# Kernel tuning notes

Hardware: AMD Instinct MI355X
Metric: run time of the kernel (lower is better)

Reference implementation:

```python
import jax, jax.numpy as jnp
import numpy as np

B, T, F = 128, 512, 64
H, OUT, NUM_LAYERS = 1024, 64, 2


def _lstm_layer(x, W_ih, W_hh, b_ih, b_hh):
    # x: [B, T, Fin]; W_ih: [4H, Fin]; W_hh: [4H, H]; b_*: [4H]
    # PyTorch gate order: i, f, g, o
    Bsz = x.shape[0]
    Hd = W_hh.shape[1]
    # Precompute input contribution for all timesteps: [B, T, 4H]
    xg = jnp.einsum('btf,gf->btg', x, W_ih) + b_ih + b_hh

    def step(carry, xg_t):
        h, c = carry
        g = xg_t + h @ W_hh.T  # [B, 4H]
        i, f, gg, o = jnp.split(g, 4, axis=-1)
        i = jax.nn.sigmoid(i)
        f = jax.nn.sigmoid(f)
        gg = jnp.tanh(gg)
        o = jax.nn.sigmoid(o)
        c = f * c + i * gg
        h = o * jnp.tanh(c)
        return (h, c), h

    h0 = jnp.zeros((Bsz, Hd), dtype=x.dtype)
    c0 = jnp.zeros((Bsz, Hd), dtype=x.dtype)
    _, hs = jax.lax.scan(step, (h0, c0), jnp.swapaxes(xg, 0, 1))  # hs: [T, B, H]
    return jnp.swapaxes(hs, 0, 1)  # [B, T, H]


def setup_inputs() -> dict:
    key = jax.random.key(0)
    ks = jax.random.split(key, 12)
    s_in = 1.0 / np.sqrt(H)
    inp = {
        'input_batch': jax.random.normal(ks[0], (B, T, F), dtype=jnp.float32),
        'W_ih0': jax.random.uniform(ks[1], (4 * H, F), minval=-s_in, maxval=s_in),
        'W_hh0': jax.random.uniform(ks[2], (4 * H, H), minval=-s_in, maxval=s_in),
        'b_ih0': jax.random.uniform(ks[3], (4 * H,), minval=-s_in, maxval=s_in),
        'b_hh0': jax.random.uniform(ks[4], (4 * H,), minval=-s_in, maxval=s_in),
        'W_ih1': jax.random.uniform(ks[5], (4 * H, H), minval=-s_in, maxval=s_in),
        'W_hh1': jax.random.uniform(ks[6], (4 * H, H), minval=-s_in, maxval=s_in),
        'b_ih1': jax.random.uniform(ks[7], (4 * H,), minval=-s_in, maxval=s_in),
        'b_hh1': jax.random.uniform(ks[8], (4 * H,), minval=-s_in, maxval=s_in),
        'W_fc': jax.random.uniform(ks[9], (OUT, H), minval=-s_in, maxval=s_in),
        'b_fc': jax.random.uniform(ks[10], (OUT,), minval=-s_in, maxval=s_in),
    }
    return inp


def reference(input_batch, W_ih0, W_hh0, b_ih0, b_hh0, W_ih1, W_hh1, b_ih1, b_hh1, W_fc, b_fc):
    # The per-timestep python loop with carried (h, c) is mathematically a full
    # sequence pass through the stacked LSTM, with the Linear applied at every step.
    h1 = _lstm_layer(input_batch, W_ih0, W_hh0, b_ih0, b_hh0)  # [B, T, H]
    h2 = _lstm_layer(h1, W_ih1, W_hh1, b_ih1, b_hh1)           # [B, T, H]
    preds = jnp.einsum('bth,oh->bto', h2, W_fc) + b_fc          # [B, T, OUT]
    return preds
```

## Files before the change

kernel.cpp:

```cpp
#include <hip/hip_runtime.h>
#include <hip/hip_bf16.h>

typedef __bf16 bf16_t;
typedef bf16_t bf16x8 __attribute__((ext_vector_type(8)));
typedef float f32x4 __attribute__((ext_vector_type(4)));
typedef unsigned long long u64;

#define T_SEQ 512
#define NB 128
#define HID 1024
#define FIN 64
#define HB (NB * HID)
#define NBLK 256
#define DM 32
#define DX 8
#define X1SLOT (4096 * NB)

#define NF0 136
#define NF1 128
#define NFR 64
#define L0_STAGE (NF0 * 64 * 8)
#define L1_STAGE (NFR * 64 * 8)
#define LDS_BYTES 151552

#define F0 0
#define FX 64
#define F1 128
#define SYNC_N 256

__device__ __forceinline__ float sigm_f(float x) { return 1.0f / (1.0f + __expf(-x)); }
__device__ __forceinline__ float tanh_f(float x) { return 2.0f * sigm_f(2.0f * x) - 1.0f; }

__device__ __forceinline__ unsigned ldcnt(const unsigned* p) {
    return __hip_atomic_load(p, __ATOMIC_RELAXED, __HIP_MEMORY_SCOPE_AGENT);
}
__device__ __forceinline__ void stw32(unsigned* p, unsigned v) {
    __hip_atomic_store(p, v, __ATOMIC_RELAXED, __HIP_MEMORY_SCOPE_AGENT);
}
__device__ __forceinline__ void stwf(float* p, float v) {
    __hip_atomic_store(p, v, __ATOMIC_RELAXED, __HIP_MEMORY_SCOPE_AGENT);
}
__device__ __forceinline__ void stw64(u64* p, u64 v) {
    __hip_atomic_store(p, v, __ATOMIC_RELAXED, __HIP_MEMORY_SCOPE_AGENT);
}


__global__ __launch_bounds__(256) void prep_kernel(
    const float* __restrict__ x,
    const float* __restrict__ Wih0, const float* __restrict__ Whh0,
    const float* __restrict__ bih0, const float* __restrict__ bhh0,
    const float* __restrict__ Wih1, const float* __restrict__ Whh1,
    const float* __restrict__ bih1, const float* __restrict__ bhh1,
    const float* __restrict__ Wfc,
    bf16_t* __restrict__ Wf0, bf16_t* __restrict__ Wf1, bf16_t* __restrict__ WfR,
    bf16_t* __restrict__ xswz, bf16_t* __restrict__ Wfcb,
    float* __restrict__ bias0, float* __restrict__ bias1,
    bf16_t* __restrict__ mh0, bf16_t* __restrict__ mh1,
    unsigned* __restrict__ sync)
{
    const unsigned stride = gridDim.x * blockDim.x;
    const unsigned i0 = blockIdx.x * blockDim.x + threadIdx.x;

    for (unsigned i = i0; i < SYNC_N; i += stride) sync[i] = 0u;

    for (unsigned i = i0; i < 64u * NF0 * 64u; i += stride) {
        unsigned g0 = i / (NF0 * 64u), rem = i % (NF0 * 64u);
        unsigned f = rem >> 6, ln = rem & 63u;
        unsigned pc = f >> 2, mt = f & 3u;
        unsigned r = mt * 16u + (ln & 15u);
        unsigned row = (r & 3u) * HID + g0 * 16u + (r >> 2);
        unsigned k0 = pc * 32u + (ln >> 4) * 8u;
        bf16_t* dst = Wf0 + (size_t)i * 8;
#pragma unroll
        for (int e = 0; e < 8; ++e) {
            unsigned k = k0 + e;
            float v = (k < FIN) ? Wih0[(size_t)row * FIN + k]
                                : Whh0[(size_t)row * HID + (k - FIN)];
            dst[e] = (bf16_t)v;
        }
    }
    for (unsigned i = i0; i < 64u * NF1 * 64u; i += stride) {
        unsigned g = i >> 13, rem = i & 8191u;
        unsigned f = rem >> 6, ln = rem & 63u;
        unsigned pc = f >> 2, mt = f & 3u;
        unsigned r = mt * 16u + (ln & 15u);
        unsigned row = (r & 3u) * HID + g * 16u + (r >> 2);
        unsigned k0 = pc * 32u + (ln >> 4) * 8u;
        bf16_t* dst = Wf1 + (size_t)i * 8;
#pragma unroll
        for (int e = 0; e < 8; ++e)
            dst[e] = (bf16_t)Wih1[(size_t)row * HID + k0 + e];
    }
    for (unsigned i = i0; i < 128u * NFR * 64u; i += stride) {
        unsigned g1 = i >> 12, rem = i & 4095u;
        unsigned f = rem >> 6, ln = rem & 63u;
        unsigned pc = f >> 1, mt = f & 1u;
        unsigned r = mt * 16u + (ln & 15u);
        unsigned row = (r & 3u) * HID + g1 * 8u + (r >> 2);
        unsigned k0 = pc * 32u + (ln >> 4) * 8u;
        bf16_t* dst = WfR + (size_t)i * 8;
#pragma unroll
        for (int e = 0; e < 8; ++e)
            dst[e] = (bf16_t)Whh1[(size_t)row * HID + k0 + e];
    }
    for (unsigned i = i0; i < 4194304u; i += stride) {
        unsigned e = i & 7u, unit = i >> 3;
        unsigned lane = unit & 63u, g = unit >> 6;
        unsigned wvv = g & 7u, pt = g >> 3;
        unsigned p = pt & 1u, t = pt >> 1;
        unsigned n = wvv * 16u + (lane & 15u);
        unsigned k = p * 32u + (lane >> 4) * 8u + e;
        xswz[i] = (bf16_t)x[((size_t)n * T_SEQ + t) * FIN + k];
    }
    for (unsigned i = i0; i < 64u * HID; i += stride)
        Wfcb[i] = (bf16_t)Wfc[i];
    for (unsigned i = i0; i < (unsigned)(DM * HB); i += stride) {
        mh0[i] = (bf16_t)0.0f; mh1[i] = (bf16_t)0.0f;
    }
    for (unsigned i = i0; i < 4096u; i += stride) {
        bias0[i] = bih0[i] + bhh0[i];
        bias1[i] = bih1[i] + bhh1[i];
    }
}

__global__ __launch_bounds__(512) void lstm_persist(
    const bf16_t* __restrict__ Wf0, const bf16_t* __restrict__ Wf1,
    const bf16_t* __restrict__ WfR,
    const float* __restrict__ bias0, const float* __restrict__ bias1,
    const bf16_t* __restrict__ xswz,
    bf16_t* __restrict__ mh0, bf16_t* __restrict__ mh1,
    bf16_t* __restrict__ h2buf,
    float* __restrict__ x1r,
    unsigned* __restrict__ sync)
{
    extern __shared__ bf16_t Wl[];
    const int b = blockIdx.x;
    const int tid = threadIdx.x;
    const int wv = tid >> 6;
    const int lane = tid & 63;
    const int q = lane >> 4;
    const int l = lane & 15;

    if (b < 64) {
        const int g0 = b;
        const int mh = wv >> 2, nh = wv & 3;
        const int nt0 = nh * 2, nt1 = nh * 2 + 1;
        for (int c = tid; c < NF0 * 64; c += 512)
            *(bf16x8*)(Wl + (size_t)c * 8) =
                *(const bf16x8*)(Wf0 + ((size_t)g0 * (NF0 * 64) + c) * 8);
        bf16_t* stage = Wl + L0_STAGE;
        float* cl = (float*)(Wl + L0_STAGE + 2048);
        for (int i = tid; i < 16 * NB; i += 512) cl[i] = 0.0f;
        float bj[2][4];
#pragma unroll
        for (int mti = 0; mti < 2; ++mti) {
            const int j = g0 * 16 + (mh * 2 + mti) * 4 + q;
#pragma unroll
            for (int gg = 0; gg < 4; ++gg) bj[mti][gg] = bias0[gg * HID + j];
        }
        __syncthreads();

        for (int t = 0; t < T_SEQ; ++t) {
            f32x4 acc[2][2] = {{{0.f,0.f,0.f,0.f},{0.f,0.f,0.f,0.f}},
                               {{0.f,0.f,0.f,0.f},{0.f,0.f,0.f,0.f}}};
            {
                const bf16_t* X = xswz + (size_t)t * 8192;
#pragma unroll
                for (int p = 0; p < 2; ++p) {
                    bf16x8 av0 = *(const bf16x8*)(Wl + ((size_t)(p * 4 + mh * 2) * 64 + lane) * 8);
                    bf16x8 av1 = *(const bf16x8*)(Wl + ((size_t)(p * 4 + mh * 2 + 1) * 64 + lane) * 8);
                    bf16x8 bv0 = *(const bf16x8*)(X + (((size_t)p * 8 + nt0) * 64 + lane) * 8);
                    bf16x8 bv1 = *(const bf16x8*)(X + (((size_t)p * 8 + nt1) * 64 + lane) * 8);
                    acc[0][0] = __builtin_amdgcn_mfma_f32_16x16x32_bf16(av0, bv0, acc[0][0], 0, 0, 0);
                    acc[0][1] = __builtin_amdgcn_mfma_f32_16x16x32_bf16(av0, bv1, acc[0][1], 0, 0, 0);
                    acc[1][0] = __builtin_amdgcn_mfma_f32_16x16x32_bf16(av1, bv0, acc[1][0], 0, 0, 0);
                    acc[1][1] = __builtin_amdgcn_mfma_f32_16x16x32_bf16(av1, bv1, acc[1][1], 0, 0, 0);
                }
            }
            if (wv == 0) {
                const unsigned tA = (unsigned)t;
                const unsigned tB = (t >= DM) ? (unsigned)(t - (DM - 1)) : 0u;
                for (;;) {
                    bool ok = (ldcnt(&sync[F0 + lane]) >= tA)
                           && (ldcnt(&sync[FX + lane]) >= tB);
                    if (__all(ok)) break;
                    __builtin_amdgcn_s_sleep(1);
                }
            }
            __syncthreads();
            {
                const bf16_t* B = mh0 + (size_t)((t + DM - 1) & (DM - 1)) * HB;
                bf16x8 bb0[8], bb1[8];
#pragma unroll
                for (int i = 0; i < 8; ++i) {
                    bb0[i] = *(const bf16x8*)(B + (((size_t)i * 8 + nt0) * 64 + lane) * 8);
                    bb1[i] = *(const bf16x8*)(B + (((size_t)i * 8 + nt1) * 64 + lane) * 8);
                }
#pragma unroll
                for (int p = 0; p < 32; ++p) {
                    bf16x8 av0 = *(const bf16x8*)(Wl + ((size_t)((2 + p) * 4 + mh * 2) * 64 + lane) * 8);
                    bf16x8 av1 = *(const bf16x8*)(Wl + ((size_t)((2 + p) * 4 + mh * 2 + 1) * 64 + lane) * 8);
                    acc[0][0] = __builtin_amdgcn_mfma_f32_16x16x32_bf16(av0, bb0[p & 7], acc[0][0], 0, 0, 0);
                    acc[0][1] = __builtin_amdgcn_mfma_f32_16x16x32_bf16(av0, bb1[p & 7], acc[0][1], 0, 0, 0);
                    acc[1][0] = __builtin_amdgcn_mfma_f32_16x16x32_bf16(av1, bb0[p & 7], acc[1][0], 0, 0, 0);
                    acc[1][1] = __builtin_amdgcn_mfma_f32_16x16x32_bf16(av1, bb1[p & 7], acc[1][1], 0, 0, 0);
                    if (p + 8 < 32) {
                        bb0[p & 7] = *(const bf16x8*)(B + (((size_t)(p + 8) * 8 + nt0) * 64 + lane) * 8);
                        bb1[p & 7] = *(const bf16x8*)(B + (((size_t)(p + 8) * 8 + nt1) * 64 + lane) * 8);
                    }
                }
            }
#pragma unroll
            for (int mti = 0; mti < 2; ++mti) {
                const int u = (mh * 2 + mti) * 4 + q;
#pragma unroll
                for (int nti = 0; nti < 2; ++nti) {
                    const int n = (nh * 2 + nti) * 16 + l;
                    float iv = sigm_f(acc[mti][nti][0] + bj[mti][0]);
                    float fv = sigm_f(acc[mti][nti][1] + bj[mti][1]);
                    float gv = tanh_f(acc[mti][nti][2] + bj[mti][2]);
                    float ov = sigm_f(acc[mti][nti][3] + bj[mti][3]);
                    float cn = fv * cl[u * NB + n] + iv * gv;
                    cl[u * NB + n] = cn;
                    stage[n * 16 + u] = (bf16_t)(ov * tanh_f(cn));
                }
            }
            __syncthreads();
            if (tid < 256) {
                const int n = tid >> 1, half = tid & 1;
                u64 v0 = *(const u64*)(stage + n * 16 + half * 8);
                u64 v1 = *(const u64*)(stage + n * 16 + half * 8 + 4);
                size_t unit = ((size_t)((g0 >> 1) * 8 + (n >> 4))) * 64
                              + ((g0 & 1) * 2 + half) * 16 + (n & 15);
                u64* dst = (u64*)(mh0 + (size_t)(t & (DM - 1)) * HB) + unit * 2;
                stw64(dst, v0); stw64(dst + 1, v1);
            }
            __syncthreads();
            if (tid == 0) stw32(&sync[F0 + g0], (unsigned)(t + 1));
        }
    } else if (b < 128) {
        const int g = b - 64;
        const int mh = wv >> 2, nh = wv & 3;
        const int nt0 = nh * 2, nt1 = nh * 2 + 1;
        for (int c = tid; c < NF1 * 64; c += 512)
            *(bf16x8*)(Wl + (size_t)c * 8) =
                *(const bf16x8*)(Wf1 + ((size_t)g * (NF1 * 64) + c) * 8);
        __syncthreads();

        for (int t = 0; t < T_SEQ; ++t) {
            if (wv == 0) {
                const unsigned tA = (unsigned)(t + 1);
                const unsigned tC = (t >= DX) ? (unsigned)(t - (DX - 1)) : 0u;
                for (;;) {
                    bool ok = (ldcnt(&sync[F0 + lane]) >= tA)
                           && (ldcnt(&sync[F1 + lane]) >= tC)
                           && (ldcnt(&sync[F1 + 64 + lane]) >= tC);
                    if (__all(ok)) break;
                    __builtin_amdgcn_s_sleep(1);
                }
            }
            __syncthreads();
            f32x4 acc[2][2] = {{{0.f,0.f,0.f,0.f},{0.f,0.f,0.f,0.f}},
                               {{0.f,0.f,0.f,0.f},{0.f,0.f,0.f,0.f}}};
            {
                const bf16_t* B = mh0 + (size_t)(t & (DM - 1)) * HB;
                bf16x8 bb0[8], bb1[8];
#pragma unroll
                for (int i = 0; i < 8; ++i) {
                    bb0[i] = *(const bf16x8*)(B + (((size_t)i * 8 + nt0) * 64 + lane) * 8);
                    bb1[i] = *(const bf16x8*)(B + (((size_t)i * 8 + nt1) * 64 + lane) * 8);
                }
#pragma unroll
                for (int p = 0; p < 32; ++p) {
                    bf16x8 av0 = *(const bf16x8*)(Wl + ((size_t)(p * 4 + mh * 2) * 64 + lane) * 8);
                    bf16x8 av1 = *(const bf16x8*)(Wl + ((size_t)(p * 4 + mh * 2 + 1) * 64 + lane) * 8);
                    acc[0][0] = __builtin_amdgcn_mfma_f32_16x16x32_bf16(av0, bb0[p & 7], acc[0][0], 0, 0, 0);
                    acc[0][1] = __builtin_amdgcn_mfma_f32_16x16x32_bf16(av0, bb1[p & 7], acc[0][1], 0, 0, 0);
                    acc[1][0] = __builtin_amdgcn_mfma_f32_16x16x32_bf16(av1, bb0[p & 7], acc[1][0], 0, 0, 0);
                    acc[1][1] = __builtin_amdgcn_mfma_f32_16x16x32_bf16(av1, bb1[p & 7], acc[1][1], 0, 0, 0);
                    if (p + 8 < 32) {
                        bb0[p & 7] = *(const bf16x8*)(B + (((size_t)(p + 8) * 8 + nt0) * 64 + lane) * 8);
                        bb1[p & 7] = *(const bf16x8*)(B + (((size_t)(p + 8) * 8 + nt1) * 64 + lane) * 8);
                    }
                }
            }
            {
                float* P = x1r + (size_t)(t & (DX - 1)) * X1SLOT + (size_t)g * 64 * NB;
#pragma unroll
                for (int mti = 0; mti < 2; ++mti) {
                    const int u = (mh * 2 + mti) * 4 + q;
#pragma unroll
                    for (int nti = 0; nti < 2; ++nti) {
                        const int n = (nh * 2 + nti) * 16 + l;
#pragma unroll
                        for (int jj = 0; jj < 4; ++jj)
                            stwf(P + (size_t)(u * 4 + jj) * NB + n, acc[mti][nti][jj]);
                    }
                }
            }
            __syncthreads();
            if (tid == 0) stw32(&sync[FX + g], (unsigned)(t + 1));
        }
    } else {
        const int g1 = b - 128;
        const int nn = wv * 16 + l;
        for (int c = tid; c < NFR * 64; c += 512)
            *(bf16x8*)(Wl + (size_t)c * 8) =
                *(const bf16x8*)(WfR + ((size_t)g1 * (NFR * 64) + c) * 8);
        bf16_t* stage = Wl + L1_STAGE;
        float* cl = (float*)(Wl + L1_STAGE + 1024);
        for (int i = tid; i < 8 * NB; i += 512) cl[i] = 0.0f;
        float bj[2][4];
#pragma unroll
        for (int mt = 0; mt < 2; ++mt) {
            const int j = g1 * 8 + mt * 4 + q;
#pragma unroll
            for (int gg = 0; gg < 4; ++gg) bj[mt][gg] = bias1[gg * HID + j];
        }
        __syncthreads();

        for (int t = 0; t < T_SEQ; ++t) {
            if (wv == 0) {
                const unsigned tA = (unsigned)(t + 1);
                const unsigned tO = (unsigned)t;
                const unsigned gx = (unsigned)(g1 >> 1);
                for (;;) {
                    bool ok = (ldcnt(&sync[FX + gx]) >= tA)
                           && (ldcnt(&sync[F1 + lane]) >= tO)
                           && (ldcnt(&sync[F1 + 64 + lane]) >= tO);
                    if (__all(ok)) break;
                    __builtin_amdgcn_s_sleep(1);
                }
            }
            __syncthreads();
            float pv[2][4];
            {
                const float* P = x1r + (size_t)(t & (DX - 1)) * X1SLOT + (size_t)g1 * 32 * NB;
#pragma unroll
                for (int mt = 0; mt < 2; ++mt)
#pragma unroll
                    for (int jj = 0; jj < 4; ++jj)
                        pv[mt][jj] = P[(size_t)((mt * 4 + q) * 4 + jj) * NB + nn];
            }
            f32x4 acc[2] = {{0.f,0.f,0.f,0.f},{0.f,0.f,0.f,0.f}};
            {
                const bf16_t* B1 = mh1 + (size_t)((t + DM - 1) & (DM - 1)) * HB;
                bf16x8 bb[16];
#pragma unroll
                for (int i = 0; i < 16; ++i)
                    bb[i] = *(const bf16x8*)(B1 + (((size_t)i * 8 + wv) * 64 + lane) * 8);
#pragma unroll
                for (int p = 0; p < 32; ++p) {
                    bf16x8 bv = bb[p & 15];
#pragma unroll
                    for (int mt = 0; mt < 2; ++mt) {
                        bf16x8 av = *(const bf16x8*)(Wl + ((size_t)(p * 2 + mt) * 64 + lane) * 8);
                        acc[mt] = __builtin_amdgcn_mfma_f32_16x16x32_bf16(av, bv, acc[mt], 0, 0, 0);
                    }
                    if (p + 16 < 32)
                        bb[p & 15] = *(const bf16x8*)(B1 + (((size_t)(p + 16) * 8 + wv) * 64 + lane) * 8);
                }
            }
#pragma unroll
            for (int mt = 0; mt < 2; ++mt) {
                const int u = mt * 4 + q;
                float iv = sigm_f(acc[mt][0] + pv[mt][0] + bj[mt][0]);
                float fv = sigm_f(acc[mt][1] + pv[mt][1] + bj[mt][1]);
                float gv = tanh_f(acc[mt][2] + pv[mt][2] + bj[mt][2]);
                float ov = sigm_f(acc[mt][3] + pv[mt][3] + bj[mt][3]);
                float cn = fv * cl[u * NB + nn] + iv * gv;
                cl[u * NB + nn] = cn;
                stage[nn * 8 + u] = (bf16_t)(ov * tanh_f(cn));
            }
            __asm__ volatile("s_waitcnt lgkmcnt(0)" ::: "memory");
            u64 v = 0;
            if (q < 2) {
                v = *(const u64*)(stage + (size_t)(wv * 16 + l) * 8 + q * 4);
                size_t unit = ((size_t)(g1 >> 2) * 8 + wv) * 64 + (size_t)(g1 & 3) * 16 + l;
                stw64((u64*)(mh1 + (size_t)(t & (DM - 1)) * HB) + unit * 2 + q, v);
            }
            __syncthreads();
            if (tid == 0) stw32(&sync[F1 + g1], (unsigned)(t + 1));
            if (q < 2)
                *(u64*)(h2buf + ((size_t)(wv * 16 + l) * T_SEQ + t) * HID + g1 * 8 + q * 4) = v;
        }
    }
}

__global__ __launch_bounds__(256) void fc_kernel(
    const bf16_t* __restrict__ h2buf, const bf16_t* __restrict__ Wfcb,
    const float* __restrict__ bfc, float* __restrict__ out)
{
    const int tid = threadIdx.x, wv = tid >> 6, lane = tid & 63;
    const int q = lane >> 4, l = lane & 15;
    const int m0 = blockIdx.x * 64 + wv * 16;
    const bf16_t* arow = h2buf + (size_t)(m0 + l) * HID + q * 8;
    const bf16_t* brow = Wfcb + (size_t)l * HID + q * 8;
    f32x4 acc[4] = {{0.f,0.f,0.f,0.f},{0.f,0.f,0.f,0.f},{0.f,0.f,0.f,0.f},{0.f,0.f,0.f,0.f}};
#pragma unroll 4
    for (int p = 0; p < 32; ++p) {
        bf16x8 av = *(const bf16x8*)(arow + p * 32);
#pragma unroll
        for (int ntile = 0; ntile < 4; ++ntile) {
            bf16x8 bv = *(const bf16x8*)(brow + (size_t)ntile * 16 * HID + p * 32);
            acc[ntile] = __builtin_amdgcn_mfma_f32_16x16x32_bf16(av, bv, acc[ntile], 0, 0, 0);
        }
    }
#pragma unroll
    for (int ntile = 0; ntile < 4; ++ntile) {
        float bv = bfc[ntile * 16 + l];
#pragma unroll
        for (int r = 0; r < 4; ++r)
            out[(size_t)(m0 + q * 4 + r) * 64 + ntile * 16 + l] = acc[ntile][r] + bv;
    }
}

extern "C" void kernel_launch(void* const* d_in, const int* in_sizes, int n_in,
                              void* d_out, int out_size, void* d_ws, size_t ws_size,
                              hipStream_t stream)
{
    const float* x    = (const float*)d_in[0];
    const float* Wih0 = (const float*)d_in[1];
    const float* Whh0 = (const float*)d_in[2];
    const float* bih0 = (const float*)d_in[3];
    const float* bhh0 = (const float*)d_in[4];
    const float* Wih1 = (const float*)d_in[5];
    const float* Whh1 = (const float*)d_in[6];
    const float* bih1 = (const float*)d_in[7];
    const float* bhh1 = (const float*)d_in[8];
    const float* Wfc  = (const float*)d_in[9];
    const float* bfc  = (const float*)d_in[10];
    float* out = (float*)d_out;

    char* ws = (char*)d_ws;
    size_t off = 0;
    auto alloc = [&](size_t bytes) -> void* {
        void* p = ws + off;
        off += (bytes + 255) & ~(size_t)255;
        return p;
    };
    bf16_t* Wf0  = (bf16_t*)alloc((size_t)64 * NF0 * 64 * 8 * 2);
    bf16_t* Wf1  = (bf16_t*)alloc((size_t)64 * NF1 * 64 * 8 * 2);
    bf16_t* WfR  = (bf16_t*)alloc((size_t)128 * NFR * 64 * 8 * 2);
    bf16_t* xswz = (bf16_t*)alloc((size_t)NB * T_SEQ * FIN * 2);
    bf16_t* h2buf= (bf16_t*)alloc((size_t)NB * T_SEQ * HID * 2);
    bf16_t* mh0  = (bf16_t*)alloc((size_t)DM * HB * 2);
    bf16_t* mh1  = (bf16_t*)alloc((size_t)DM * HB * 2);
    float*  x1r  = (float*)alloc((size_t)DX * X1SLOT * 4);
    float*  bias0= (float*)alloc(4096 * 4);
    float*  bias1= (float*)alloc(4096 * 4);
    bf16_t* Wfcb = (bf16_t*)alloc((size_t)64 * HID * 2);
    unsigned* syncp = (unsigned*)alloc(SYNC_N * 4);
    if (off > ws_size) return;

    hipFuncSetAttribute((const void*)lstm_persist,
                        hipFuncAttributeMaxDynamicSharedMemorySize, LDS_BYTES);

    prep_kernel<<<1024, 256, 0, stream>>>(x, Wih0, Whh0, bih0, bhh0,
                                          Wih1, Whh1, bih1, bhh1, Wfc,
                                          Wf0, Wf1, WfR, xswz, Wfcb,
                                          bias0, bias1, mh0, mh1, syncp);

    void* args[] = { (void*)&Wf0, (void*)&Wf1, (void*)&WfR,
                     (void*)&bias0, (void*)&bias1,
                     (void*)&xswz, (void*)&mh0, (void*)&mh1,
                     (void*)&h2buf, (void*)&x1r,
                     (void*)&syncp };
    hipLaunchCooperativeKernel((void*)lstm_persist, dim3(NBLK), dim3(512),
                               args, LDS_BYTES, stream);

    fc_kernel<<<(NB * T_SEQ) / 64, 256, 0, stream>>>(h2buf, Wfcb, bfc, out);
}
```

Measured before the change: 4.817 ms.

## Split batch into two independent half-chunks pipelined through the persistent LSTM

```diff
diff --git a/kernel.cpp b/kernel.cpp
--- a/kernel.cpp
+++ b/kernel.cpp
@@ -10,11 +10,11 @@
 #define NB 128
 #define HID 1024
 #define FIN 64
-#define HB (NB * HID)
+#define HBH (64 * 1024)
 #define NBLK 256
 #define DM 32
 #define DX 8
-#define X1SLOT (4096 * NB)
+#define X1SLOTH (4096 * 64)
 
 #define NF0 136
 #define NF1 128
@@ -23,10 +23,7 @@
 #define L1_STAGE (NFR * 64 * 8)
 #define LDS_BYTES 151552
 
-#define F0 0
-#define FX 64
-#define F1 128
-#define SYNC_N 256
+#define SYNC_N 512
 
 __device__ __forceinline__ float sigm_f(float x) { return 1.0f / (1.0f + __expf(-x)); }
 __device__ __forceinline__ float tanh_f(float x) { return 2.0f * sigm_f(2.0f * x) - 1.0f; }
@@ -106,15 +103,14 @@
     for (unsigned i = i0; i < 4194304u; i += stride) {
         unsigned e = i & 7u, unit = i >> 3;
         unsigned lane = unit & 63u, g = unit >> 6;
-        unsigned wvv = g & 7u, pt = g >> 3;
-        unsigned p = pt & 1u, t = pt >> 1;
-        unsigned n = wvv * 16u + (lane & 15u);
+        unsigned nt = g & 3u, p = (g >> 2) & 1u, c = (g >> 3) & 1u, t = g >> 4;
+        unsigned n = c * 64u + nt * 16u + (lane & 15u);
         unsigned k = p * 32u + (lane >> 4) * 8u + e;
         xswz[i] = (bf16_t)x[((size_t)n * T_SEQ + t) * FIN + k];
     }
     for (unsigned i = i0; i < 64u * HID; i += stride)
         Wfcb[i] = (bf16_t)Wfc[i];
-    for (unsigned i = i0; i < (unsigned)(DM * HB); i += stride) {
+    for (unsigned i = i0; i < (unsigned)(2 * DM * HBH); i += stride) {
         mh0[i] = (bf16_t)0.0f; mh1[i] = (bf16_t)0.0f;
     }
     for (unsigned i = i0; i < 4096u; i += stride) {
@@ -123,7 +119,7 @@
     }
 }
 
-__global__ __launch_bounds__(512) void lstm_persist(
+__global__ __launch_bounds__(512, 2) void lstm_persist(
     const bf16_t* __restrict__ Wf0, const bf16_t* __restrict__ Wf1,
     const bf16_t* __restrict__ WfR,
     const float* __restrict__ bias0, const float* __restrict__ bias1,
@@ -140,16 +136,16 @@
     const int lane = tid & 63;
     const int q = lane >> 4;
     const int l = lane & 15;
+    const int mh = wv >> 2;
+    const int nh = wv & 3;
 
     if (b < 64) {
         const int g0 = b;
-        const int mh = wv >> 2, nh = wv & 3;
-        const int nt0 = nh * 2, nt1 = nh * 2 + 1;
-        for (int c = tid; c < NF0 * 64; c += 512)
-            *(bf16x8*)(Wl + (size_t)c * 8) =
-                *(const bf16x8*)(Wf0 + ((size_t)g0 * (NF0 * 64) + c) * 8);
+        for (int cc = tid; cc < NF0 * 64; cc += 512)
+            *(bf16x8*)(Wl + (size_t)cc * 8) =
+                *(const bf16x8*)(Wf0 + ((size_t)g0 * (NF0 * 64) + cc) * 8);
         bf16_t* stage = Wl + L0_STAGE;
-        float* cl = (float*)(Wl + L0_STAGE + 2048);
+        float* cl = (float*)(Wl + L0_STAGE + 1024);
         for (int i = tid; i < 16 * NB; i += 512) cl[i] = 0.0f;
         float bj[2][4];
 #pragma unroll
@@ -161,228 +157,212 @@
         __syncthreads();
 
         for (int t = 0; t < T_SEQ; ++t) {
-            f32x4 acc[2][2] = {{{0.f,0.f,0.f,0.f},{0.f,0.f,0.f,0.f}},
-                               {{0.f,0.f,0.f,0.f},{0.f,0.f,0.f,0.f}}};
-            {
-                const bf16_t* X = xswz + (size_t)t * 8192;
-#pragma unroll
-                for (int p = 0; p < 2; ++p) {
-                    bf16x8 av0 = *(const bf16x8*)(Wl + ((size_t)(p * 4 + mh * 2) * 64 + lane) * 8);
-                    bf16x8 av1 = *(const bf16x8*)(Wl + ((size_t)(p * 4 + mh * 2 + 1) * 64 + lane) * 8);
-                    bf16x8 bv0 = *(const bf16x8*)(X + (((size_t)p * 8 + nt0) * 64 + lane) * 8);
-                    bf16x8 bv1 = *(const bf16x8*)(X + (((size_t)p * 8 + nt1) * 64 + lane) * 8);
-                    acc[0][0] = __builtin_amdgcn_mfma_f32_16x16x32_bf16(av0, bv0, acc[0][0], 0, 0, 0);
-                    acc[0][1] = __builtin_amdgcn_mfma_f32_16x16x32_bf16(av0, bv1, acc[0][1], 0, 0, 0);
-                    acc[1][0] = __builtin_amdgcn_mfma_f32_16x16x32_bf16(av1, bv0, acc[1][0], 0, 0, 0);
-                    acc[1][1] = __builtin_amdgcn_mfma_f32_16x16x32_bf16(av1, bv1, acc[1][1], 0, 0, 0);
-                }
+#pragma unroll
+            for (int c = 0; c < 2; ++c) {
+                f32x4 acc[2] = {{0.f,0.f,0.f,0.f},{0.f,0.f,0.f,0.f}};
+                {
+                    const bf16_t* X = xswz + (size_t)(t * 2 + c) * 4096;
+#pragma unroll
+                    for (int p = 0; p < 2; ++p) {
+                        bf16x8 bv  = *(const bf16x8*)(X + (((size_t)p * 4 + nh) * 64 + lane) * 8);
+                        bf16x8 av0 = *(const bf16x8*)(Wl + ((size_t)(p * 4 + mh * 2) * 64 + lane) * 8);
+                        bf16x8 av1 = *(const bf16x8*)(Wl + ((size_t)(p * 4 + mh * 2 + 1) * 64 + lane) * 8);
+                        acc[0] = __builtin_amdgcn_mfma_f32_16x16x32_bf16(av0, bv, acc[0], 0, 0, 0);
+                        acc[1] = __builtin_amdgcn_mfma_f32_16x16x32_bf16(av1, bv, acc[1], 0, 0, 0);
+                    }
+                }
+                if (wv == 0) {
+                    const unsigned tA = (unsigned)t;
+                    const unsigned tB = (t >= DM) ? (unsigned)(t - (DM - 1)) : 0u;
+                    const unsigned* f0c = sync + c * 64;
+                    const unsigned* fxc = sync + 128 + c * 64;
+                    for (;;) {
+                        bool ok = (ldcnt(&f0c[lane]) >= tA) && (ldcnt(&fxc[lane]) >= tB);
+                        if (__all(ok)) break;
+                        __builtin_amdgcn_s_sleep(1);
+                    }
+                }
+                __syncthreads();
+                {
+                    const bf16_t* B = mh0 + ((size_t)c * DM + ((t + DM - 1) & (DM - 1))) * HBH;
+                    bf16x8 bb[16];
+#pragma unroll
+                    for (int i = 0; i < 16; ++i)
+                        bb[i] = *(const bf16x8*)(B + (((size_t)i * 4 + nh) * 64 + lane) * 8);
+#pragma unroll
+                    for (int p = 0; p < 32; ++p) {
+                        bf16x8 av0 = *(const bf16x8*)(Wl + ((size_t)((2 + p) * 4 + mh * 2) * 64 + lane) * 8);
+                        bf16x8 av1 = *(const bf16x8*)(Wl + ((size_t)((2 + p) * 4 + mh * 2 + 1) * 64 + lane) * 8);
+                        acc[0] = __builtin_amdgcn_mfma_f32_16x16x32_bf16(av0, bb[p & 15], acc[0], 0, 0, 0);
+                        acc[1] = __builtin_amdgcn_mfma_f32_16x16x32_bf16(av1, bb[p & 15], acc[1], 0, 0, 0);
+                        if (p + 16 < 32)
+                            bb[p & 15] = *(const bf16x8*)(B + (((size_t)(p + 16) * 4 + nh) * 64 + lane) * 8);
+                    }
+                }
+#pragma unroll
+                for (int mti = 0; mti < 2; ++mti) {
+                    const int u = (mh * 2 + mti) * 4 + q;
+                    const int n = nh * 16 + l;
+                    float iv = sigm_f(acc[mti][0] + bj[mti][0]);
+                    float fv = sigm_f(acc[mti][1] + bj[mti][1]);
+                    float gv = tanh_f(acc[mti][2] + bj[mti][2]);
+                    float ov = sigm_f(acc[mti][3] + bj[mti][3]);
+                    const int ci = u * NB + c * 64 + n;
+                    float cn = fv * cl[ci] + iv * gv;
+                    cl[ci] = cn;
+                    stage[n * 16 + u] = (bf16_t)(ov * tanh_f(cn));
+                }
+                __asm__ volatile("s_waitcnt lgkmcnt(0)" ::: "memory");
+                if (q < 2) {
+                    const int ug = mh * 2 + q;
+                    const int n = nh * 16 + l;
+                    u64 v = *(const u64*)(stage + n * 16 + ug * 4);
+                    const int j0 = g0 * 16 + ug * 4;
+                    size_t unit = (((size_t)(j0 >> 5)) * 4 + nh) * 64 + ((j0 >> 3) & 3) * 16 + l;
+                    u64* ring = (u64*)(mh0 + ((size_t)c * DM + (t & (DM - 1))) * HBH);
+                    stw64(ring + unit * 2 + ((j0 & 7) >> 2), v);
+                }
+                __syncthreads();
+                if (tid == 0) stw32(&sync[c * 64 + g0], (unsigned)(t + 1));
             }
-            if (wv == 0) {
-                const unsigned tA = (unsigned)t;
-                const unsigned tB = (t >= DM) ? (unsigned)(t - (DM - 1)) : 0u;
-                for (;;) {
-                    bool ok = (ldcnt(&sync[F0 + lane]) >= tA)
-                           && (ldcnt(&sync[FX + lane]) >= tB);
-                    if (__all(ok)) break;
-                    __builtin_amdgcn_s_sleep(1);
-                }
-            }
-            __syncthreads();
-            {
-                const bf16_t* B = mh0 + (size_t)((t + DM - 1) & (DM - 1)) * HB;
-                bf16x8 bb0[8], bb1[8];
-#pragma unroll
-                for (int i = 0; i < 8; ++i) {
-                    bb0[i] = *(const bf16x8*)(B + (((size_t)i * 8 + nt0) * 64 + lane) * 8);
-                    bb1[i] = *(const bf16x8*)(B + (((size_t)i * 8 + nt1) * 64 + lane) * 8);
-                }
-#pragma unroll
-                for (int p = 0; p < 32; ++p) {
-                    bf16x8 av0 = *(const bf16x8*)(Wl + ((size_t)((2 + p) * 4 + mh * 2) * 64 + lane) * 8);
-                    bf16x8 av1 = *(const bf16x8*)(Wl + ((size_t)((2 + p) * 4 + mh * 2 + 1) * 64 + lane) * 8);
-                    acc[0][0] = __builtin_amdgcn_mfma_f32_16x16x32_bf16(av0, bb0[p & 7], acc[0][0], 0, 0, 0);
-                    acc[0][1] = __builtin_amdgcn_mfma_f32_16x16x32_bf16(av0, bb1[p & 7], acc[0][1], 0, 0, 0);
-                    acc[1][0] = __builtin_amdgcn_mfma_f32_16x16x32_bf16(av1, bb0[p & 7], acc[1][0], 0, 0, 0);
-                    acc[1][1] = __builtin_amdgcn_mfma_f32_16x16x32_bf16(av1, bb1[p & 7], acc[1][1], 0, 0, 0);
-                    if (p + 8 < 32) {
-                        bb0[p & 7] = *(const bf16x8*)(B + (((size_t)(p + 8) * 8 + nt0) * 64 + lane) * 8);
-                        bb1[p & 7] = *(const bf16x8*)(B + (((size_t)(p + 8) * 8 + nt1) * 64 + lane) * 8);
-                    }
-                }
-            }
-#pragma unroll
-            for (int mti = 0; mti < 2; ++mti) {
-                const int u = (mh * 2 + mti) * 4 + q;
-#pragma unroll
-                for (int nti = 0; nti < 2; ++nti) {
-                    const int n = (nh * 2 + nti) * 16 + l;
-                    float iv = sigm_f(acc[mti][nti][0] + bj[mti][0]);
-                    float fv = sigm_f(acc[mti][nti][1] + bj[mti][1]);
-                    float gv = tanh_f(acc[mti][nti][2] + bj[mti][2]);
-                    float ov = sigm_f(acc[mti][nti][3] + bj[mti][3]);
-                    float cn = fv * cl[u * NB + n] + iv * gv;
-                    cl[u * NB + n] = cn;
-                    stage[n * 16 + u] = (bf16_t)(ov * tanh_f(cn));
-                }
-            }
-            __syncthreads();
-            if (tid < 256) {
-                const int n = tid >> 1, half = tid & 1;
-                u64 v0 = *(const u64*)(stage + n * 16 + half * 8);
-                u64 v1 = *(const u64*)(stage + n * 16 + half * 8 + 4);
-                size_t unit = ((size_t)((g0 >> 1) * 8 + (n >> 4))) * 64
-                              + ((g0 & 1) * 2 + half) * 16 + (n & 15);
-                u64* dst = (u64*)(mh0 + (size_t)(t & (DM - 1)) * HB) + unit * 2;
-                stw64(dst, v0); stw64(dst + 1, v1);
-            }
-            __syncthreads();
-            if (tid == 0) stw32(&sync[F0 + g0], (unsigned)(t + 1));
         }
     } else if (b < 128) {
         const int g = b - 64;
-        const int mh = wv >> 2, nh = wv & 3;
-        const int nt0 = nh * 2, nt1 = nh * 2 + 1;
-        for (int c = tid; c < NF1 * 64; c += 512)
-            *(bf16x8*)(Wl + (size_t)c * 8) =
-                *(const bf16x8*)(Wf1 + ((size_t)g * (NF1 * 64) + c) * 8);
+        for (int cc = tid; cc < NF1 * 64; cc += 512)
+            *(bf16x8*)(Wl + (size_t)cc * 8) =
+                *(const bf16x8*)(Wf1 + ((size_t)g * (NF1 * 64) + cc) * 8);
         __syncthreads();
 
         for (int t = 0; t < T_SEQ; ++t) {
-            if (wv == 0) {
-                const unsigned tA = (unsigned)(t + 1);
-                const unsigned tC = (t >= DX) ? (unsigned)(t - (DX - 1)) : 0u;
-                for (;;) {
-                    bool ok = (ldcnt(&sync[F0 + lane]) >= tA)
-                           && (ldcnt(&sync[F1 + lane]) >= tC)
-                           && (ldcnt(&sync[F1 + 64 + lane]) >= tC);
-                    if (__all(ok)) break;
-                    __builtin_amdgcn_s_sleep(1);
-                }
+#pragma unroll
+            for (int c = 0; c < 2; ++c) {
+                if (wv == 0) {
+                    const unsigned tA = (unsigned)(t + 1);
+                    const unsigned tC = (t >= DX) ? (unsigned)(t - (DX - 1)) : 0u;
+                    const unsigned* f0c = sync + c * 64;
+                    const unsigned* f1c = sync + 256 + c * 128;
+                    for (;;) {
+                        bool ok = (ldcnt(&f0c[lane]) >= tA)
+                               && (ldcnt(&f1c[lane]) >= tC)
+                               && (ldcnt(&f1c[64 + lane]) >= tC);
+                        if (__all(ok)) break;
+                        __builtin_amdgcn_s_sleep(1);
+                    }
+                }
+                __syncthreads();
+                f32x4 acc[2] = {{0.f,0.f,0.f,0.f},{0.f,0.f,0.f,0.f}};
+                {
+                    const bf16_t* B = mh0 + ((size_t)c * DM + (t & (DM - 1))) * HBH;
+                    bf16x8 bb[16];
+#pragma unroll
+                    for (int i = 0; i < 16; ++i)
+                        bb[i] = *(const bf16x8*)(B + (((size_t)i * 4 + nh) * 64 + lane) * 8);
+#pragma unroll
+                    for (int p = 0; p < 32; ++p) {
+                        bf16x8 av0 = *(const bf16x8*)(Wl + ((size_t)(p * 4 + mh * 2) * 64 + lane) * 8);
+                        bf16x8 av1 = *(const bf16x8*)(Wl + ((size_t)(p * 4 + mh * 2 + 1) * 64 + lane) * 8);
+                        acc[0] = __builtin_amdgcn_mfma_f32_16x16x32_bf16(av0, bb[p & 15], acc[0], 0, 0, 0);
+                        acc[1] = __builtin_amdgcn_mfma_f32_16x16x32_bf16(av1, bb[p & 15], acc[1], 0, 0, 0);
+                        if (p + 16 < 32)
+                            bb[p & 15] = *(const bf16x8*)(B + (((size_t)(p + 16) * 4 + nh) * 64 + lane) * 8);
+                    }
+                }
+                {
+                    float* P = x1r + ((size_t)c * DX + (t & (DX - 1))) * X1SLOTH + (size_t)g * 64 * 64;
+                    const int n = nh * 16 + l;
+#pragma unroll
+                    for (int mti = 0; mti < 2; ++mti) {
+                        const int u = (mh * 2 + mti) * 4 + q;
+#pragma unroll
+                        for (int jj = 0; jj < 4; ++jj)
+                            stwf(P + (size_t)(u * 4 + jj) * 64 + n, acc[mti][jj]);
+                    }
+                }
+                __syncthreads();
+                if (tid == 0) stw32(&sync[128 + c * 64 + g], (unsigned)(t + 1));
             }
-            __syncthreads();
-            f32x4 acc[2][2] = {{{0.f,0.f,0.f,0.f},{0.f,0.f,0.f,0.f}},
-                               {{0.f,0.f,0.f,0.f},{0.f,0.f,0.f,0.f}}};
-            {
-                const bf16_t* B = mh0 + (size_t)(t & (DM - 1)) * HB;
-                bf16x8 bb0[8], bb1[8];
-#pragma unroll
-                for (int i = 0; i < 8; ++i) {
-                    bb0[i] = *(const bf16x8*)(B + (((size_t)i * 8 + nt0) * 64 + lane) * 8);
-                    bb1[i] = *(const bf16x8*)(B + (((size_t)i * 8 + nt1) * 64 + lane) * 8);
-                }
-#pragma unroll
-                for (int p = 0; p < 32; ++p) {
-                    bf16x8 av0 = *(const bf16x8*)(Wl + ((size_t)(p * 4 + mh * 2) * 64 + lane) * 8);
-                    bf16x8 av1 = *(const bf16x8*)(Wl + ((size_t)(p * 4 + mh * 2 + 1) * 64 + lane) * 8);
-                    acc[0][0] = __builtin_amdgcn_mfma_f32_16x16x32_bf16(av0, bb0[p & 7], acc[0][0], 0, 0, 0);
-                    acc[0][1] = __builtin_amdgcn_mfma_f32_16x16x32_bf16(av0, bb1[p & 7], acc[0][1], 0, 0, 0);
-                    acc[1][0] = __builtin_amdgcn_mfma_f32_16x16x32_bf16(av1, bb0[p & 7], acc[1][0], 0, 0, 0);
-                    acc[1][1] = __builtin_amdgcn_mfma_f32_16x16x32_bf16(av1, bb1[p & 7], acc[1][1], 0, 0, 0);
-                    if (p + 8 < 32) {
-                        bb0[p & 7] = *(const bf16x8*)(B + (((size_t)(p + 8) * 8 + nt0) * 64 + lane) * 8);
-                        bb1[p & 7] = *(const bf16x8*)(B + (((size_t)(p + 8) * 8 + nt1) * 64 + lane) * 8);
-                    }
-                }
-            }
-            {
-                float* P = x1r + (size_t)(t & (DX - 1)) * X1SLOT + (size_t)g * 64 * NB;
-#pragma unroll
-                for (int mti = 0; mti < 2; ++mti) {
-                    const int u = (mh * 2 + mti) * 4 + q;
-#pragma unroll
-                    for (int nti = 0; nti < 2; ++nti) {
-                        const int n = (nh * 2 + nti) * 16 + l;
-#pragma unroll
-                        for (int jj = 0; jj < 4; ++jj)
-                            stwf(P + (size_t)(u * 4 + jj) * NB + n, acc[mti][nti][jj]);
-                    }
-                }
-            }
-            __syncthreads();
-            if (tid == 0) stw32(&sync[FX + g], (unsigned)(t + 1));
         }
     } else {
         const int g1 = b - 128;
-        const int nn = wv * 16 + l;
-        for (int c = tid; c < NFR * 64; c += 512)
-            *(bf16x8*)(Wl + (size_t)c * 8) =
-                *(const bf16x8*)(WfR + ((size_t)g1 * (NFR * 64) + c) * 8);
+        for (int cc = tid; cc < NFR * 64; cc += 512)
+            *(bf16x8*)(Wl + (size_t)cc * 8) =
+                *(const bf16x8*)(WfR + ((size_t)g1 * (NFR * 64) + cc) * 8);
         bf16_t* stage = Wl + L1_STAGE;
-        float* cl = (float*)(Wl + L1_STAGE + 1024);
+        float* cl = (float*)(Wl + L1_STAGE + 512);
         for (int i = tid; i < 8 * NB; i += 512) cl[i] = 0.0f;
-        float bj[2][4];
-#pragma unroll
-        for (int mt = 0; mt < 2; ++mt) {
-            const int j = g1 * 8 + mt * 4 + q;
-#pragma unroll
-            for (int gg = 0; gg < 4; ++gg) bj[mt][gg] = bias1[gg * HID + j];
+        float bj[4];
+        {
+            const int j = g1 * 8 + mh * 4 + q;
+#pragma unroll
+            for (int gg = 0; gg < 4; ++gg) bj[gg] = bias1[gg * HID + j];
         }
         __syncthreads();
 
         for (int t = 0; t < T_SEQ; ++t) {
-            if (wv == 0) {
-                const unsigned tA = (unsigned)(t + 1);
-                const unsigned tO = (unsigned)t;
-                const unsigned gx = (unsigned)(g1 >> 1);
-                for (;;) {
-                    bool ok = (ldcnt(&sync[FX + gx]) >= tA)
-                           && (ldcnt(&sync[F1 + lane]) >= tO)
-                           && (ldcnt(&sync[F1 + 64 + lane]) >= tO);
-                    if (__all(ok)) break;
-                    __builtin_amdgcn_s_sleep(1);
-                }
+#pragma unroll
+            for (int c = 0; c < 2; ++c) {
+                if (wv == 0) {
+                    const unsigned tA = (unsigned)(t + 1);
+                    const unsigned tO = (unsigned)t;
+                    const unsigned* fxc = sync + 128 + c * 64;
+                    const unsigned* f1c = sync + 256 + c * 128;
+                    const unsigned gx = (unsigned)(g1 >> 1);
+                    for (;;) {
+                        bool ok = (ldcnt(&fxc[gx]) >= tA)
+                               && (ldcnt(&f1c[lane]) >= tO)
+                               && (ldcnt(&f1c[64 + lane]) >= tO);
+                        if (__all(ok)) break;
+                        __builtin_amdgcn_s_sleep(1);
+                    }
+                }
+                __syncthreads();
+                float pv[4];
+                {
+                    const float* P = x1r + ((size_t)c * DX + (t & (DX - 1))) * X1SLOTH + (size_t)g1 * 32 * 64;
+#pragma unroll
+                    for (int jj = 0; jj < 4; ++jj)
+                        pv[jj] = P[(size_t)((mh * 4 + q) * 4 + jj) * 64 + nh * 16 + l];
+                }
+                f32x4 acc = {0.f, 0.f, 0.f, 0.f};
+                {
+                    const bf16_t* B = mh1 + ((size_t)c * DM + ((t + DM - 1) & (DM - 1))) * HBH;
+                    bf16x8 bb[16];
+#pragma unroll
+                    for (int i = 0; i < 16; ++i)
+                        bb[i] = *(const bf16x8*)(B + (((size_t)i * 4 + nh) * 64 + lane) * 8);
+#pragma unroll
+                    for (int p = 0; p < 32; ++p) {
+                        bf16x8 av = *(const bf16x8*)(Wl + ((size_t)(p * 2 + mh) * 64 + lane) * 8);
+                        acc = __builtin_amdgcn_mfma_f32_16x16x32_bf16(av, bb[p & 15], acc, 0, 0, 0);
+                        if (p + 16 < 32)
+                            bb[p & 15] = *(const bf16x8*)(B + (((size_t)(p + 16) * 4 + nh) * 64 + lane) * 8);
+                    }
+                }
+                {
+                    const int u = mh * 4 + q;
+                    const int n = nh * 16 + l;
+                    float iv = sigm_f(acc[0] + pv[0] + bj[0]);
+                    float fv = sigm_f(acc[1] + pv[1] + bj[1]);
+                    float gv = tanh_f(acc[2] + pv[2] + bj[2]);
+                    float ov = sigm_f(acc[3] + pv[3] + bj[3]);
+                    const int ci = u * NB + c * 64 + n;
+                    float cn = fv * cl[ci] + iv * gv;
+                    cl[ci] = cn;
+                    stage[n * 8 + u] = (bf16_t)(ov * tanh_f(cn));
+                }
+                __asm__ volatile("s_waitcnt lgkmcnt(0)" ::: "memory");
+                if (q == 0) {
+                    const int n = nh * 16 + l;
+                    u64 v = *(const u64*)(stage + n * 8 + mh * 4);
+                    const int j0 = g1 * 8 + mh * 4;
+                    size_t unit = (((size_t)(j0 >> 5)) * 4 + nh) * 64 + ((j0 >> 3) & 3) * 16 + l;
+                    u64* ring = (u64*)(mh1 + ((size_t)c * DM + (t & (DM - 1))) * HBH);
+                    stw64(ring + unit * 2 + ((j0 & 7) >> 2), v);
+                    *(u64*)(h2buf + ((size_t)(c * 64 + n) * T_SEQ + t) * HID + g1 * 8 + mh * 4) = v;
+                }
+                __syncthreads();
+                if (tid == 0) stw32(&sync[256 + c * 128 + g1], (unsigned)(t + 1));
             }
-            __syncthreads();
-            float pv[2][4];
-            {
-                const float* P = x1r + (size_t)(t & (DX - 1)) * X1SLOT + (size_t)g1 * 32 * NB;
-#pragma unroll
-                for (int mt = 0; mt < 2; ++mt)
-#pragma unroll
-                    for (int jj = 0; jj < 4; ++jj)
-                        pv[mt][jj] = P[(size_t)((mt * 4 + q) * 4 + jj) * NB + nn];
-            }
-            f32x4 acc[2] = {{0.f,0.f,0.f,0.f},{0.f,0.f,0.f,0.f}};
-            {
-                const bf16_t* B1 = mh1 + (size_t)((t + DM - 1) & (DM - 1)) * HB;
-                bf16x8 bb[16];
-#pragma unroll
-                for (int i = 0; i < 16; ++i)
-                    bb[i] = *(const bf16x8*)(B1 + (((size_t)i * 8 + wv) * 64 + lane) * 8);
-#pragma unroll
-                for (int p = 0; p < 32; ++p) {
-                    bf16x8 bv = bb[p & 15];
-#pragma unroll
-                    for (int mt = 0; mt < 2; ++mt) {
-                        bf16x8 av = *(const bf16x8*)(Wl + ((size_t)(p * 2 + mt) * 64 + lane) * 8);
-                        acc[mt] = __builtin_amdgcn_mfma_f32_16x16x32_bf16(av, bv, acc[mt], 0, 0, 0);
-                    }
-                    if (p + 16 < 32)
-                        bb[p & 15] = *(const bf16x8*)(B1 + (((size_t)(p + 16) * 8 + wv) * 64 + lane) * 8);
-                }
-            }
-#pragma unroll
-            for (int mt = 0; mt < 2; ++mt) {
-                const int u = mt * 4 + q;
-                float iv = sigm_f(acc[mt][0] + pv[mt][0] + bj[mt][0]);
-                float fv = sigm_f(acc[mt][1] + pv[mt][1] + bj[mt][1]);
-                float gv = tanh_f(acc[mt][2] + pv[mt][2] + bj[mt][2]);
-                float ov = sigm_f(acc[mt][3] + pv[mt][3] + bj[mt][3]);
-                float cn = fv * cl[u * NB + nn] + iv * gv;
-                cl[u * NB + nn] = cn;
-                stage[nn * 8 + u] = (bf16_t)(ov * tanh_f(cn));
-            }
-            __asm__ volatile("s_waitcnt lgkmcnt(0)" ::: "memory");
-            u64 v = 0;
-            if (q < 2) {
-                v = *(const u64*)(stage + (size_t)(wv * 16 + l) * 8 + q * 4);
-                size_t unit = ((size_t)(g1 >> 2) * 8 + wv) * 64 + (size_t)(g1 & 3) * 16 + l;
-                stw64((u64*)(mh1 + (size_t)(t & (DM - 1)) * HB) + unit * 2 + q, v);
-            }
-            __syncthreads();
-            if (tid == 0) stw32(&sync[F1 + g1], (unsigned)(t + 1));
-            if (q < 2)
-                *(u64*)(h2buf + ((size_t)(wv * 16 + l) * T_SEQ + t) * HID + g1 * 8 + q * 4) = v;
         }
     }
 }
@@ -444,9 +424,9 @@
     bf16_t* WfR  = (bf16_t*)alloc((size_t)128 * NFR * 64 * 8 * 2);
     bf16_t* xswz = (bf16_t*)alloc((size_t)NB * T_SEQ * FIN * 2);
     bf16_t* h2buf= (bf16_t*)alloc((size_t)NB * T_SEQ * HID * 2);
-    bf16_t* mh0  = (bf16_t*)alloc((size_t)DM * HB * 2);
-    bf16_t* mh1  = (bf16_t*)alloc((size_t)DM * HB * 2);
-    float*  x1r  = (float*)alloc((size_t)DX * X1SLOT * 4);
+    bf16_t* mh0  = (bf16_t*)alloc((size_t)2 * DM * HBH * 2);
+    bf16_t* mh1  = (bf16_t*)alloc((size_t)2 * DM * HBH * 2);
+    float*  x1r  = (float*)alloc((size_t)2 * DX * X1SLOTH * 4);
     float*  bias0= (float*)alloc(4096 * 4);
     float*  bias1= (float*)alloc(4096 * 4);
     bf16_t* Wfcb = (bf16_t*)alloc((size_t)64 * HID * 2);
```

Measured after the change: 5.148 ms. 1.07x slower.
